# Optimization experiments

Measured on AMD Instinct MI355X. Metric: run time of the kernel, lower is better.

Reference implementation:

```python
import jax, jax.numpy as jnp
import numpy as np

N = 4096
INPUT_DIM = 256
HIDDEN = 64
HEADS = 8
NEG_SLOPE = 0.2
MASK_FILL = -10000.0


def setup_inputs() -> dict:
    key = jax.random.key(0)
    k_x, k_adj, k_w, k_as, k_ad = jax.random.split(key, 5)
    x = jax.random.normal(k_x, (N, INPUT_DIM), dtype=jnp.float32)
    adjacency = jax.random.bernoulli(k_adj, 0.05, (N, N)) | jnp.eye(N, dtype=bool)
    # linear weight, torch convention: [out_features, in_features]
    W = jax.random.normal(k_w, (HEADS * HIDDEN, INPUT_DIM), dtype=jnp.float32) * 0.05
    attn_src = jax.random.normal(k_as, (HEADS, HIDDEN), dtype=jnp.float32) * 0.1
    attn_dst = jax.random.normal(k_ad, (HEADS, HIDDEN), dtype=jnp.float32) * 0.1
    return {"x": x, "adjacency": adjacency, "W": W, "attn_src": attn_src, "attn_dst": attn_dst}


def reference(x, adjacency, W, attn_src, attn_dst):
    # h: [N, heads, hidden]
    h = (x @ W.T).reshape(N, HEADS, HIDDEN)
    src_scores = jnp.einsum('nhd,hd->nh', h, attn_src)  # [N, heads]
    dst_scores = jnp.einsum('nhd,hd->nh', h, attn_dst)  # [N, heads]
    # logits[i, j, h] = src[i, h] + dst[j, h]  (matches torch permute(2,0,1) layout math)
    logits = src_scores[:, None, :] + dst_scores[None, :, :]  # [N, N, heads]
    logits = jax.nn.leaky_relu(logits, negative_slope=NEG_SLOPE)
    logits = jnp.where(adjacency[:, :, None], logits, MASK_FILL)
    alpha = jax.nn.softmax(logits, axis=1)  # softmax over source nodes j
    out = jnp.einsum('ijh,jhf->ihf', alpha, h)  # [N, heads, hidden]
    return out.mean(axis=1)  # [N, hidden]
```

## Files before the change

### kernel.cpp

```cpp
#include <hip/hip_runtime.h>

#define NN 4096
#define IN_DIM 256
#define HID 64
#define HEADS 8

typedef __attribute__((ext_vector_type(4))) float f32x4;
typedef __attribute__((ext_vector_type(8))) short s16x8;
typedef unsigned short u16;
typedef unsigned long long u64;

__device__ inline u16 f2bf(float f) {
  union { float f; unsigned u; } v; v.f = f;
  unsigned r = (v.u + 0x7FFFu + ((v.u >> 16) & 1u)) >> 16;
  return (u16)r;
}
__device__ inline float bf2f(u16 b) {
  union { unsigned u; float f; } v; v.u = ((unsigned)b) << 16;
  return v.f;
}
__device__ __forceinline__ unsigned cvt_pk_bf16(float a, float b) {
  unsigned r;
  asm("v_cvt_pk_bf16_f32 %0, %1, %2" : "=v"(r) : "v"(a), "v"(b));
  return r;
}

__global__ void gat_detect(const void* __restrict__ adj, int* __restrict__ flag)
{
  const int lane = threadIdx.x;
  const unsigned char* a8 = (const unsigned char*)adj;
  const int* a32 = (const int*)adj;

  size_t i8 = (size_t)(4 * lane + 1) * 4097;
  int p8 = a8[i8] != 0;

  size_t k = (size_t)(2 * lane + 1);
  int p32 = a32[k * 4097] != 0;
  int p64 = a32[2 * k * 4097] != 0;

  int ok8 = __all(p8), ok32 = __all(p32), ok64 = __all(p64);
  if (lane == 0) *flag = ok8 ? 0 : (ok32 ? 1 : (ok64 ? 2 : 1));
}

__global__ __launch_bounds__(256) void gat_pack(
    const void* __restrict__ adj, const int* __restrict__ flag,
    u64* __restrict__ bits)
{
  const int mode = *flag;
  const int lane = threadIdx.x & 63;
  const int wave = (blockIdx.x * blockDim.x + threadIdx.x) >> 6;
  const int nwaves = (gridDim.x * blockDim.x) >> 6;
  const size_t nwords = (size_t)NN * NN / 64;

  for (size_t w = wave; w < nwords; w += nwaves) {
    size_t e = w * 64 + lane;
    int on;
    if (mode == 1)      on = ((const int*)adj)[e] != 0;
    else if (mode == 0) on = ((const unsigned char*)adj)[e] != 0;
    else                on = ((const long long*)adj)[e] != 0;
    u64 b = __ballot(on);
    if (lane == 0) bits[w] = b;
  }
}

__global__ __launch_bounds__(256) void gat_gemm1(
    const float* __restrict__ x, const float* __restrict__ W,
    float* __restrict__ Hf, u16* __restrict__ Hbt)
{
  __shared__ u16 xhi[64 * 72], xlo[64 * 72], whi[64 * 72], wlo[64 * 72];
  const int nb = blockIdx.x;
  const int ob = blockIdx.y;
  const int t = threadIdx.x;
  const int lane = t & 63, wid = t >> 6;
  const int wr = wid >> 1, wc = wid & 1;
  const int g = lane >> 4;

  f32x4 acc[2][2] = {};

  const int sn = t >> 2;
  const int skc = (t & 3) * 16;

  for (int kb = 0; kb < 4; ++kb) {
    const float* xr = x + (size_t)(nb * 64 + sn) * IN_DIM + kb * 64 + skc;
    const float* wr_p = W + (size_t)(ob * 64 + sn) * IN_DIM + kb * 64 + skc;
#pragma unroll
    for (int c = 0; c < 4; ++c) {
      float4 xv = ((const float4*)xr)[c];
      float4 wv = ((const float4*)wr_p)[c];
      float xf[4] = {xv.x, xv.y, xv.z, xv.w};
      float wf[4] = {wv.x, wv.y, wv.z, wv.w};
      u16 xh[4], xl[4], wh[4], wl[4];
#pragma unroll
      for (int e = 0; e < 4; ++e) {
        xh[e] = f2bf(xf[e]); xl[e] = f2bf(xf[e] - bf2f(xh[e]));
        wh[e] = f2bf(wf[e]); wl[e] = f2bf(wf[e] - bf2f(wh[e]));
      }
      int base = sn * 72 + skc + c * 4;
      *(ushort4*)(xhi + base) = make_ushort4(xh[0], xh[1], xh[2], xh[3]);
      *(ushort4*)(xlo + base) = make_ushort4(xl[0], xl[1], xl[2], xl[3]);
      *(ushort4*)(whi + base) = make_ushort4(wh[0], wh[1], wh[2], wh[3]);
      *(ushort4*)(wlo + base) = make_ushort4(wl[0], wl[1], wl[2], wl[3]);
    }
    __syncthreads();
#pragma unroll
    for (int ks = 0; ks < 2; ++ks) {
      const int k0 = ks * 32 + g * 8;
      s16x8 ah[2], al[2], bh[2], bl[2];
#pragma unroll
      for (int nf = 0; nf < 2; ++nf) {
        int row = wr * 32 + nf * 16 + (lane & 15);
        ah[nf] = *(const s16x8*)(xhi + row * 72 + k0);
        al[nf] = *(const s16x8*)(xlo + row * 72 + k0);
      }
#pragma unroll
      for (int of = 0; of < 2; ++of) {
        int row = wc * 32 + of * 16 + (lane & 15);
        bh[of] = *(const s16x8*)(whi + row * 72 + k0);
        bl[of] = *(const s16x8*)(wlo + row * 72 + k0);
      }
#pragma unroll
      for (int nf = 0; nf < 2; ++nf)
#pragma unroll
        for (int of = 0; of < 2; ++of) {
          acc[nf][of] = __builtin_amdgcn_mfma_f32_16x16x32_bf16(ah[nf], bh[of], acc[nf][of], 0, 0, 0);
          acc[nf][of] = __builtin_amdgcn_mfma_f32_16x16x32_bf16(ah[nf], bl[of], acc[nf][of], 0, 0, 0);
          acc[nf][of] = __builtin_amdgcn_mfma_f32_16x16x32_bf16(al[nf], bh[of], acc[nf][of], 0, 0, 0);
        }
    }
    __syncthreads();
  }

#pragma unroll
  for (int nf = 0; nf < 2; ++nf)
#pragma unroll
    for (int of = 0; of < 2; ++of)
#pragma unroll
      for (int r = 0; r < 4; ++r) {
        int nloc = wr * 32 + nf * 16 + g * 4 + r;
        int oloc = wc * 32 + of * 16 + (lane & 15);
        Hf[(size_t)(nb * 64 + nloc) * 512 + ob * 64 + oloc] = acc[nf][of][r];
      }
  u16* Ct = xhi;
#pragma unroll
  for (int nf = 0; nf < 2; ++nf)
#pragma unroll
    for (int of = 0; of < 2; ++of)
#pragma unroll
      for (int r = 0; r < 4; ++r) {
        int nloc = wr * 32 + nf * 16 + g * 4 + r;
        int oloc = wc * 32 + of * 16 + (lane & 15);
        Ct[oloc * 72 + nloc] = f2bf(acc[nf][of][r]);
      }
  __syncthreads();
  {
    int o = t >> 2, nc = (t & 3) * 16;
    u16* dst = Hbt + ((size_t)(ob * 64 + nb) * 64 + o) * 64 + nc;
#pragma unroll
    for (int c = 0; c < 2; ++c) {
      s16x8 v = *(const s16x8*)(Ct + o * 72 + nc + c * 8);
      *(s16x8*)(dst + c * 8) = v;
    }
  }
}

__global__ __launch_bounds__(256) void gat_scores(
    const float* __restrict__ Hf, const float* __restrict__ a_src,
    const float* __restrict__ a_dst, float* __restrict__ s_srcT,
    float* __restrict__ s_dstT)
{
  int node = blockIdx.x * 4 + (threadIdx.x >> 6);
  int lane = threadIdx.x & 63;
  int h = lane >> 3, c = lane & 7;
  const float* hrow = Hf + (size_t)node * 512 + h * 64 + c * 8;
  const float* as = a_src + h * 64 + c * 8;
  const float* ad = a_dst + h * 64 + c * 8;
  float vs = 0.f, vd = 0.f;
#pragma unroll
  for (int e = 0; e < 8; ++e) { float hv = hrow[e]; vs += hv * as[e]; vd += hv * ad[e]; }
#pragma unroll
  for (int m = 1; m < 8; m <<= 1) { vs += __shfl_xor(vs, m); vd += __shfl_xor(vd, m); }
  if (c == 0) { s_srcT[h * NN + node] = vs; s_dstT[h * NN + node] = vd; }
}

__global__ __launch_bounds__(512) void gat_dmax(
    const float* __restrict__ s_dstT, float* __restrict__ Mh)
{
  const int w = threadIdx.x >> 6, lane = threadIdx.x & 63;
  const float* p = s_dstT + (size_t)w * NN;
  float m = -INFINITY;
#pragma unroll
  for (int it = 0; it < 16; ++it) {
    f32x4 v = *(const f32x4*)(p + (it * 64 + lane) * 4);
    m = fmaxf(fmaxf(fmaxf(m, v[0]), v[1]), fmaxf(v[2], v[3]));
  }
#pragma unroll
  for (int s = 1; s < 64; s <<= 1) m = fmaxf(m, __shfl_xor(m, s));
  if (lane == 0) Mh[w] = m;
}

__global__ __launch_bounds__(256, 2) void gat_flash(
    const u64* __restrict__ bits, const u16* __restrict__ Hbt,
    const float* __restrict__ s_srcT, const float* __restrict__ s_dstT,
    const float* __restrict__ Mh, float* __restrict__ pout)
{
  __shared__ u16 Ast[4096];

  const int t = threadIdx.x, lane = t & 63, wid = t >> 6;
  const int bid = blockIdx.x;
  const int h = bid & 7, iblk = bid >> 3;
  const int i_loc = lane & 15, g = lane >> 4, j0 = g * 8;
  const int irow = iblk * 64 + wid * 16 + i_loc;

  const float s_i = s_srcT[(size_t)h * NN + irow];
  float m_i = s_i + Mh[h];
  m_i = fmaxf(m_i, 0.2f * m_i);
  const float L2E = 1.44269504f;
  const float mL = m_i * L2E;

  const u16* tile0 = Hbt + (size_t)h * 64 * 4096;
  const float* dT = s_dstT + (size_t)h * NN;
  const u64* brow = bits + (size_t)irow * 64;

  const int r0 = t >> 3, colE = (t & 7) * 8;
  const u16* gsrc0 = tile0 + r0 * 64 + (colE ^ ((r0 & 7) << 3));
  const int r1 = 32 + r0;
  const u16* gsrc1 = tile0 + r1 * 64 + (colE ^ ((r1 & 7) << 3));

  const int swz = (i_loc & 7) << 4;
  const char* lbase = (const char*)Ast;

  f32x4 acc[4] = {};
  f32x4 lacc = {0.f, 0.f, 0.f, 0.f};

#define QUAD(DV, MBITS, SH, PW0, PW1, LI) do {                        \
    float z0 = s_i + DV[0], z1 = s_i + DV[1];                         \
    float z2 = s_i + DV[2], z3 = s_i + DV[3];                         \
    z0 = fmaxf(z0, 0.2f * z0); z1 = fmaxf(z1, 0.2f * z1);             \
    z2 = fmaxf(z2, 0.2f * z2); z3 = fmaxf(z3, 0.2f * z3);             \
    float e0 = __builtin_amdgcn_exp2f(__builtin_fmaf(z0, L2E, -mL));  \
    float e1 = __builtin_amdgcn_exp2f(__builtin_fmaf(z1, L2E, -mL));  \
    float e2 = __builtin_amdgcn_exp2f(__builtin_fmaf(z2, L2E, -mL));  \
    float e3 = __builtin_amdgcn_exp2f(__builtin_fmaf(z3, L2E, -mL));  \
    e0 = ((MBITS >> (SH + 0)) & 1u) ? e0 : 0.f;                       \
    e1 = ((MBITS >> (SH + 1)) & 1u) ? e1 : 0.f;                       \
    e2 = ((MBITS >> (SH + 2)) & 1u) ? e2 : 0.f;                       \
    e3 = ((MBITS >> (SH + 3)) & 1u) ? e3 : 0.f;                       \
    lacc[LI] += (e0 + e1) + (e2 + e3);                                \
    PW0 = cvt_pk_bf16(e0, e1); PW1 = cvt_pk_bf16(e2, e3);             \
  } while (0)

  u64 am_n = brow[0];
  f32x4 d_n0 = *(const f32x4*)(dT + j0);
  f32x4 d_n1 = *(const f32x4*)(dT + j0 + 4);
  f32x4 d_n2 = *(const f32x4*)(dT + 32 + j0);
  f32x4 d_n3 = *(const f32x4*)(dT + 36 + j0);

  for (int jt = 0; jt < 64; ++jt) {
    s16x8 sv0 = *(const s16x8*)(gsrc0 + jt * 4096);
    s16x8 sv1 = *(const s16x8*)(gsrc1 + jt * 4096);

    const u64 am_ = am_n;
    f32x4 d0 = d_n0, d1 = d_n1, d2 = d_n2, d3 = d_n3;
    const int jn = (jt + 1 < 64) ? jt + 1 : 63;
    am_n = brow[jn];
    d_n0 = *(const f32x4*)(dT + jn * 64 + j0);
    d_n1 = *(const f32x4*)(dT + jn * 64 + j0 + 4);
    d_n2 = *(const f32x4*)(dT + jn * 64 + 32 + j0);
    d_n3 = *(const f32x4*)(dT + jn * 64 + 36 + j0);

    const unsigned amlo = (unsigned)(am_ >> j0);
    const unsigned amhi = (unsigned)(am_ >> (32 + j0));
    union { unsigned w_[4]; s16x8 v_; } P0, P1;
    QUAD(d0, amlo, 0, P0.w_[0], P0.w_[1], 0);
    QUAD(d1, amlo, 4, P0.w_[2], P0.w_[3], 1);
    QUAD(d2, amhi, 0, P1.w_[0], P1.w_[1], 2);
    QUAD(d3, amhi, 4, P1.w_[2], P1.w_[3], 3);

    __syncthreads();
    *(s16x8*)(Ast + t * 8) = sv0;
    *(s16x8*)(Ast + 2048 + t * 8) = sv1;
    __syncthreads();

#pragma unroll
    for (int fb = 0; fb < 4; ++fb) {
      const int rowb = (fb * 16 + i_loc) * 128;
      s16x8 A0 = *(const s16x8*)(lbase + rowb + ((g * 16) ^ swz));
      s16x8 A1 = *(const s16x8*)(lbase + rowb + (((g * 16) + 64) ^ swz));
      acc[fb] = __builtin_amdgcn_mfma_f32_16x16x32_bf16(A0, P0.v_, acc[fb], 0, 0, 0);
      acc[fb] = __builtin_amdgcn_mfma_f32_16x16x32_bf16(A1, P1.v_, acc[fb], 0, 0, 0);
    }
  }
#undef QUAD

  float l_run = (lacc[0] + lacc[1]) + (lacc[2] + lacc[3]);
  l_run += __shfl_xor(l_run, 16);
  l_run += __shfl_xor(l_run, 32);
  const float invL = 1.f / l_run;

  float* ob = pout + ((size_t)h * NN + irow) * 64;
#pragma unroll
  for (int fb = 0; fb < 4; ++fb) {
    f32x4 v = acc[fb] * invL;
    *(f32x4*)(ob + fb * 16 + g * 4) = v;
  }
}

__global__ __launch_bounds__(256) void gat_combine(
    const float* __restrict__ pout, float* __restrict__ out)
{
  size_t e = (size_t)blockIdx.x * 256 + threadIdx.x;
  f32x4 s = {0.f, 0.f, 0.f, 0.f};
#pragma unroll
  for (int h = 0; h < 8; ++h)
    s += ((const f32x4*)pout)[(size_t)h * (NN * 16) + e];
  ((f32x4*)out)[e] = s * 0.125f;
}

extern "C" void kernel_launch(void* const* d_in, const int* in_sizes, int n_in,
                              void* d_out, int out_size, void* d_ws, size_t ws_size,
                              hipStream_t stream)
{
  const float* x = (const float*)d_in[0];
  const void* adj = d_in[1];
  const float* W = (const float*)d_in[2];
  const float* a_src = (const float*)d_in[3];
  const float* a_dst = (const float*)d_in[4];
  float* out = (float*)d_out;

  char* ws = (char*)d_ws;
  float* Hf = (float*)ws;
  u16* Hbt = (u16*)(ws + 8 * 1024 * 1024);
  float* s_srcT = (float*)(ws + 12 * 1024 * 1024);
  float* s_dstT = (float*)(ws + 12 * 1024 * 1024 + 128 * 1024);
  int* flag = (int*)(ws + 12 * 1024 * 1024 + 256 * 1024);
  float* Mh = (float*)(ws + 12 * 1024 * 1024 + 384 * 1024);
  u64* bits = (u64*)(ws + 12 * 1024 * 1024 + 512 * 1024);
  float* pout = (float*)ws;

  gat_detect<<<1, 64, 0, stream>>>(adj, flag);
  gat_pack<<<2048, 256, 0, stream>>>(adj, flag, bits);
  gat_gemm1<<<dim3(64, 8), 256, 0, stream>>>(x, W, Hf, Hbt);
  gat_scores<<<1024, 256, 0, stream>>>(Hf, a_src, a_dst, s_srcT, s_dstT);
  gat_dmax<<<1, 512, 0, stream>>>(s_dstT, Mh);
  gat_flash<<<512, 256, 0, stream>>>(bits, Hbt, s_srcT, s_dstT, Mh, pout);
  gat_combine<<<256, 256, 0, stream>>>(pout, out);
}
```

Measured before the change: 110.4 us.

## Fuse attention scores into GEMM epilogue and split flash j-range across wave groups

The per-head source and destination attention scores are now computed in the GEMM epilogue by shuffle-reducing the accumulators against a_src/a_dst. This removes the fp32 H write and the separate gat_scores kernel. The flash kernel now runs 512 threads per block, and two groups of four waves each process half of the 64 j-tiles. Their partial accumulators and row sums are merged through shared memory before normalisation. This doubles the waves available per output tile to hide latency, at the cost of an extra LDS merge, more barriers and higher LDS use per block.

```diff
diff --git a/kernel.cpp b/kernel.cpp
--- a/kernel.cpp
+++ b/kernel.cpp
@@ -65,7 +65,9 @@
 
 __global__ __launch_bounds__(256) void gat_gemm1(
     const float* __restrict__ x, const float* __restrict__ W,
-    float* __restrict__ Hf, u16* __restrict__ Hbt)
+    const float* __restrict__ a_src, const float* __restrict__ a_dst,
+    u16* __restrict__ Hbt, float* __restrict__ s_srcT,
+    float* __restrict__ s_dstT)
 {
   __shared__ u16 xhi[64 * 72], xlo[64 * 72], whi[64 * 72], wlo[64 * 72];
   const int nb = blockIdx.x;
@@ -130,16 +132,6 @@
     __syncthreads();
   }
 
-#pragma unroll
-  for (int nf = 0; nf < 2; ++nf)
-#pragma unroll
-    for (int of = 0; of < 2; ++of)
-#pragma unroll
-      for (int r = 0; r < 4; ++r) {
-        int nloc = wr * 32 + nf * 16 + g * 4 + r;
-        int oloc = wc * 32 + of * 16 + (lane & 15);
-        Hf[(size_t)(nb * 64 + nloc) * 512 + ob * 64 + oloc] = acc[nf][of][r];
-      }
   u16* Ct = xhi;
 #pragma unroll
   for (int nf = 0; nf < 2; ++nf)
@@ -151,6 +143,28 @@
         int oloc = wc * 32 + of * 16 + (lane & 15);
         Ct[oloc * 72 + nloc] = f2bf(acc[nf][of][r]);
       }
+
+  {
+    const float* asp = a_src + ob * 64;
+    const float* adp = a_dst + ob * 64;
+    float as0 = asp[wc * 32 + (lane & 15)], as1 = asp[wc * 32 + 16 + (lane & 15)];
+    float ad0 = adp[wc * 32 + (lane & 15)], ad1 = adp[wc * 32 + 16 + (lane & 15)];
+    float* sred = (float*)wlo;
+#pragma unroll
+    for (int nf = 0; nf < 2; ++nf)
+#pragma unroll
+      for (int r = 0; r < 4; ++r) {
+        float vs = acc[nf][0][r] * as0 + acc[nf][1][r] * as1;
+        float vd = acc[nf][0][r] * ad0 + acc[nf][1][r] * ad1;
+#pragma unroll
+        for (int m = 1; m < 16; m <<= 1) { vs += __shfl_xor(vs, m); vd += __shfl_xor(vd, m); }
+        if ((lane & 15) == 0) {
+          int node = wr * 32 + nf * 16 + g * 4 + r;
+          sred[wc * 64 + node] = vs;
+          sred[128 + wc * 64 + node] = vd;
+        }
+      }
+  }
   __syncthreads();
   {
     int o = t >> 2, nc = (t & 3) * 16;
@@ -161,25 +175,11 @@
       *(s16x8*)(dst + c * 8) = v;
     }
   }
-}
-
-__global__ __launch_bounds__(256) void gat_scores(
-    const float* __restrict__ Hf, const float* __restrict__ a_src,
-    const float* __restrict__ a_dst, float* __restrict__ s_srcT,
-    float* __restrict__ s_dstT)
-{
-  int node = blockIdx.x * 4 + (threadIdx.x >> 6);
-  int lane = threadIdx.x & 63;
-  int h = lane >> 3, c = lane & 7;
-  const float* hrow = Hf + (size_t)node * 512 + h * 64 + c * 8;
-  const float* as = a_src + h * 64 + c * 8;
-  const float* ad = a_dst + h * 64 + c * 8;
-  float vs = 0.f, vd = 0.f;
-#pragma unroll
-  for (int e = 0; e < 8; ++e) { float hv = hrow[e]; vs += hv * as[e]; vd += hv * ad[e]; }
-#pragma unroll
-  for (int m = 1; m < 8; m <<= 1) { vs += __shfl_xor(vs, m); vd += __shfl_xor(vd, m); }
-  if (c == 0) { s_srcT[h * NN + node] = vs; s_dstT[h * NN + node] = vd; }
+  if (t < 64) {
+    const float* sred = (const float*)wlo;
+    s_srcT[(size_t)ob * NN + nb * 64 + t] = sred[t] + sred[64 + t];
+    s_dstT[(size_t)ob * NN + nb * 64 + t] = sred[128 + t] + sred[192 + t];
+  }
 }
 
 __global__ __launch_bounds__(512) void gat_dmax(
@@ -198,18 +198,22 @@
   if (lane == 0) Mh[w] = m;
 }
 
-__global__ __launch_bounds__(256, 2) void gat_flash(
+__global__ __launch_bounds__(512, 4) void gat_flash(
     const u64* __restrict__ bits, const u16* __restrict__ Hbt,
     const float* __restrict__ s_srcT, const float* __restrict__ s_dstT,
     const float* __restrict__ Mh, float* __restrict__ pout)
 {
-  __shared__ u16 Ast[4096];
+  __shared__ char shmem[17408];
+  __shared__ float Lbuf[8][16];
+  u16* Ast = (u16*)shmem;
+  float (*Mbuf)[16][66] = (float(*)[16][66])shmem;
 
   const int t = threadIdx.x, lane = t & 63, wid = t >> 6;
+  const int ws4 = wid & 3, jh = wid >> 2;
   const int bid = blockIdx.x;
   const int h = bid & 7, iblk = bid >> 3;
   const int i_loc = lane & 15, g = lane >> 4, j0 = g * 8;
-  const int irow = iblk * 64 + wid * 16 + i_loc;
+  const int irow = iblk * 64 + ws4 * 16 + i_loc;
 
   const float s_i = s_srcT[(size_t)h * NN + irow];
   float m_i = s_i + Mh[h];
@@ -221,13 +225,14 @@
   const float* dT = s_dstT + (size_t)h * NN;
   const u64* brow = bits + (size_t)irow * 64;
 
-  const int r0 = t >> 3, colE = (t & 7) * 8;
+  const int lt = t & 255;
+  const int r0 = lt >> 3, colE = (lt & 7) * 8;
   const u16* gsrc0 = tile0 + r0 * 64 + (colE ^ ((r0 & 7) << 3));
   const int r1 = 32 + r0;
   const u16* gsrc1 = tile0 + r1 * 64 + (colE ^ ((r1 & 7) << 3));
-
+  u16* sdst = Ast + jh * 4096;
+  const char* lbase = (const char*)(Ast + jh * 4096);
   const int swz = (i_loc & 7) << 4;
-  const char* lbase = (const char*)Ast;
 
   f32x4 acc[4] = {};
   f32x4 lacc = {0.f, 0.f, 0.f, 0.f};
@@ -249,19 +254,21 @@
     PW0 = cvt_pk_bf16(e0, e1); PW1 = cvt_pk_bf16(e2, e3);             \
   } while (0)
 
-  u64 am_n = brow[0];
-  f32x4 d_n0 = *(const f32x4*)(dT + j0);
-  f32x4 d_n1 = *(const f32x4*)(dT + j0 + 4);
-  f32x4 d_n2 = *(const f32x4*)(dT + 32 + j0);
-  f32x4 d_n3 = *(const f32x4*)(dT + 36 + j0);
-
-  for (int jt = 0; jt < 64; ++jt) {
+  const int jt0 = jh * 32;
+  u64 am_n = brow[jt0];
+  f32x4 d_n0 = *(const f32x4*)(dT + jt0 * 64 + j0);
+  f32x4 d_n1 = *(const f32x4*)(dT + jt0 * 64 + j0 + 4);
+  f32x4 d_n2 = *(const f32x4*)(dT + jt0 * 64 + 32 + j0);
+  f32x4 d_n3 = *(const f32x4*)(dT + jt0 * 64 + 36 + j0);
+
+  for (int it = 0; it < 32; ++it) {
+    const int jt = jt0 + it;
     s16x8 sv0 = *(const s16x8*)(gsrc0 + jt * 4096);
     s16x8 sv1 = *(const s16x8*)(gsrc1 + jt * 4096);
 
     const u64 am_ = am_n;
     f32x4 d0 = d_n0, d1 = d_n1, d2 = d_n2, d3 = d_n3;
-    const int jn = (jt + 1 < 64) ? jt + 1 : 63;
+    const int jn = jt0 + ((it + 1 < 32) ? it + 1 : 31);
     am_n = brow[jn];
     d_n0 = *(const f32x4*)(dT + jn * 64 + j0);
     d_n1 = *(const f32x4*)(dT + jn * 64 + j0 + 4);
@@ -277,8 +284,8 @@
     QUAD(d3, amhi, 4, P1.w_[2], P1.w_[3], 3);
 
     __syncthreads();
-    *(s16x8*)(Ast + t * 8) = sv0;
-    *(s16x8*)(Ast + 2048 + t * 8) = sv1;
+    *(s16x8*)(sdst + lt * 8) = sv0;
+    *(s16x8*)(sdst + 2048 + lt * 8) = sv1;
     __syncthreads();
 
 #pragma unroll
@@ -295,13 +302,23 @@
   float l_run = (lacc[0] + lacc[1]) + (lacc[2] + lacc[3]);
   l_run += __shfl_xor(l_run, 16);
   l_run += __shfl_xor(l_run, 32);
-  const float invL = 1.f / l_run;
-
-  float* ob = pout + ((size_t)h * NN + irow) * 64;
-#pragma unroll
-  for (int fb = 0; fb < 4; ++fb) {
-    f32x4 v = acc[fb] * invL;
-    *(f32x4*)(ob + fb * 16 + g * 4) = v;
+  if (lane < 16) Lbuf[wid][i_loc] = l_run;
+
+  __syncthreads();
+  if (jh == 1) {
+#pragma unroll
+    for (int fb = 0; fb < 4; ++fb)
+      *(f32x4*)&Mbuf[ws4][i_loc][fb * 16 + g * 4] = acc[fb];
+  }
+  __syncthreads();
+  if (jh == 0) {
+    const float invL = 1.f / (l_run + Lbuf[wid + 4][i_loc]);
+    float* ob = pout + ((size_t)h * NN + irow) * 64;
+#pragma unroll
+    for (int fb = 0; fb < 4; ++fb) {
+      f32x4 v = (acc[fb] + *(const f32x4*)&Mbuf[ws4][i_loc][fb * 16 + g * 4]) * invL;
+      *(f32x4*)(ob + fb * 16 + g * 4) = v;
+    }
   }
 }
 
@@ -328,20 +345,18 @@
   float* out = (float*)d_out;
 
   char* ws = (char*)d_ws;
-  float* Hf = (float*)ws;
+  float* pout = (float*)ws;
   u16* Hbt = (u16*)(ws + 8 * 1024 * 1024);
   float* s_srcT = (float*)(ws + 12 * 1024 * 1024);
   float* s_dstT = (float*)(ws + 12 * 1024 * 1024 + 128 * 1024);
   int* flag = (int*)(ws + 12 * 1024 * 1024 + 256 * 1024);
   float* Mh = (float*)(ws + 12 * 1024 * 1024 + 384 * 1024);
   u64* bits = (u64*)(ws + 12 * 1024 * 1024 + 512 * 1024);
-  float* pout = (float*)ws;
 
   gat_detect<<<1, 64, 0, stream>>>(adj, flag);
   gat_pack<<<2048, 256, 0, stream>>>(adj, flag, bits);
-  gat_gemm1<<<dim3(64, 8), 256, 0, stream>>>(x, W, Hf, Hbt);
-  gat_scores<<<1024, 256, 0, stream>>>(Hf, a_src, a_dst, s_srcT, s_dstT);
+  gat_gemm1<<<dim3(64, 8), 256, 0, stream>>>(x, W, a_src, a_dst, Hbt, s_srcT, s_dstT);
   gat_dmax<<<1, 512, 0, stream>>>(s_dstT, Mh);
-  gat_flash<<<512, 256, 0, stream>>>(bits, Hbt, s_srcT, s_dstT, Mh, pout);
+  gat_flash<<<512, 512, 0, stream>>>(bits, Hbt, s_srcT, s_dstT, Mh, pout);
   gat_combine<<<256, 256, 0, stream>>>(pout, out);
 }
```

After: 100.3 us. 9.2% less time.
